# Optimization experiments

Measured on AMD Instinct MI355X. Metric: run time of the kernel, lower is better.

The kernel has to match this reference:

```python
import jax, jax.numpy as jnp
from jax import lax
import numpy as np

K = 48          # dim_embedding_key
PAST = 20
FUT = 40
N = 65536       # total surrounding-agent nodes
E = 1048576     # edges
B = 1           # batch (structurally forced to 1 by the original code)


def conv1d_relu(x, w, b):
    # x: [B, 2, T], w: [K, 2, 3], padding=1 -> relu(Conv1d)
    y = lax.conv_general_dilated(x, w, (1,), ((1, 1),),
                                 dimension_numbers=('NCH', 'OIH', 'NCH'))
    return jax.nn.relu(y + b[None, :, None])


def gru_cell(xt, h, Wih, Whh, bih, bhh):
    gi = xt @ Wih.T + bih
    gh = h @ Whh.T + bhh
    ir, iz, inn = jnp.split(gi, 3, axis=-1)
    hr, hz, hn = jnp.split(gh, 3, axis=-1)
    r = jax.nn.sigmoid(ir + hr)
    z = jax.nn.sigmoid(iz + hz)
    n = jnp.tanh(inn + r * hn)
    return (1 - z) * n + z * h


def gru_last(x, Wih, Whh, bih, bhh):
    # x: [Nb, T, Din]; returns final hidden state [Nb, H] (torch GRU, h0 = 0)
    h0 = jnp.zeros((x.shape[0], Whh.shape[1]), x.dtype)
    def step(h, xt):
        h2 = gru_cell(xt, h, Wih, Whh, bih, bhh)
        return h2, None
    hT, _ = lax.scan(step, h0, jnp.swapaxes(x, 0, 1))
    return hT


def gcn_conv(x, row, col, w, W, b, n):
    # PyG GCNConv(normalize=True): add self loops (weight 1), symmetric norm,
    # x @ W.T, gather at source `row`, scatter-add at target `col`, + bias.
    loop = jnp.arange(n)
    row = jnp.concatenate([row, loop])
    col = jnp.concatenate([col, loop])
    w = jnp.concatenate([w, jnp.ones((n,), w.dtype)])
    deg = jax.ops.segment_sum(w, col, num_segments=n)
    dinv = jnp.where(deg > 0, lax.rsqrt(jnp.where(deg > 0, deg, 1.0)), 0.0)
    norm = dinv[row] * w * dinv[col]
    xw = x @ W.T
    msg = xw[row] * norm[:, None]
    return jax.ops.segment_sum(msg, col, num_segments=n) + b


def forward(past, future, x, edge_index, edge_weight,
            conv_past_w, conv_past_b, conv_fut_w, conv_fut_b,
            enc_past_Wih, enc_past_Whh, enc_past_bih, enc_past_bhh,
            enc_fut_Wih, enc_fut_Whh, enc_fut_bih, enc_fut_bhh,
            dec_Wih, dec_Whh, dec_bih, dec_bhh,
            fc_w, fc_b, gcn1_w, gcn1_b, gcn2_w, gcn2_b):
    present0 = past[:, -1, :2]                                  # [B, 2]

    # --- surrounding agents: conv1d + GRU encoder over all N nodes ---
    inter_past = jnp.swapaxes(x.reshape(-1, PAST, 2), 1, 2)     # [N, 2, T]
    story_embed = jnp.swapaxes(conv1d_relu(inter_past, conv_past_w, conv_past_b), 1, 2)
    state_past = gru_last(story_embed, enc_past_Wih, enc_past_Whh, enc_past_bih, enc_past_bhh)  # [N, K]

    # --- GCN interaction (edge_weight nonempty branch); dropout is eval-mode identity ---
    ei = edge_index.reshape(2, -1)
    ew = edge_weight.reshape(-1)
    x1 = jax.nn.relu(gcn_conv(state_past, ei[0], ei[1], ew, gcn1_w, gcn1_b, N))
    x1 = gcn_conv(x1, ei[0], ei[1], ew, gcn2_w, gcn2_b, N)
    interact_past = x1[0].reshape(B, -1)                        # [B, K] (B == 1)

    # --- ego past / future encoders ---
    past_embed = jnp.swapaxes(conv1d_relu(jnp.swapaxes(past, 1, 2), conv_past_w, conv_past_b), 1, 2)
    fut_embed = jnp.swapaxes(conv1d_relu(jnp.swapaxes(future, 1, 2), conv_fut_w, conv_fut_b), 1, 2)
    target_past = gru_last(past_embed, enc_past_Wih, enc_past_Whh, enc_past_bih, enc_past_bhh)   # [B, K]
    state_fut = gru_last(fut_embed, enc_fut_Wih, enc_fut_Whh, enc_fut_bih, enc_fut_bhh)          # [B, K]

    state_conc = jnp.concatenate([interact_past, target_past, state_fut], axis=-1)               # [B, 3K]

    zeros_in = jnp.zeros_like(state_conc)
    def step(carry, i):
        h, present = carry
        inp = jnp.where(i == 0, state_conc, zeros_in)
        h = gru_cell(inp, h, dec_Wih, dec_Whh, dec_bih, dec_bhh)
        coords = present + h @ fc_w.T + fc_b
        return (h, coords), coords
    (_, _), coords_seq = lax.scan(step, (jnp.zeros((B, 3 * K), past.dtype), present0), jnp.arange(FUT))
    return jnp.swapaxes(coords_seq, 0, 1)                        # [B, FUT, 2]


def setup_inputs() -> dict:
    ks = jax.random.split(jax.random.key(0), 32)
    def p(k, shape, s=0.1):
        return jax.random.normal(k, shape, jnp.float32) * s
    inp = {
        'past': p(ks[0], (B, PAST, 2), 1.0),
        'future': p(ks[1], (B, FUT, 2), 1.0),
        'x': p(ks[2], (N, PAST, 2), 1.0),
        'edge_index': jax.random.randint(ks[3], (1, 2, E), 0, N, jnp.int32),
        'edge_weight': jax.random.uniform(ks[4], (1, E), jnp.float32),
        'conv_past_w': p(ks[5], (K, 2, 3)), 'conv_past_b': p(ks[6], (K,)),
        'conv_fut_w': p(ks[7], (K, 2, 3)), 'conv_fut_b': p(ks[8], (K,)),
        'enc_past_Wih': p(ks[9], (3 * K, K)), 'enc_past_Whh': p(ks[10], (3 * K, K)),
        'enc_past_bih': p(ks[11], (3 * K,)), 'enc_past_bhh': p(ks[12], (3 * K,)),
        'enc_fut_Wih': p(ks[13], (3 * K, K)), 'enc_fut_Whh': p(ks[14], (3 * K, K)),
        'enc_fut_bih': p(ks[15], (3 * K,)), 'enc_fut_bhh': p(ks[16], (3 * K,)),
        'dec_Wih': p(ks[17], (9 * K, 3 * K)), 'dec_Whh': p(ks[18], (9 * K, 3 * K)),
        'dec_bih': p(ks[19], (9 * K,)), 'dec_bhh': p(ks[20], (9 * K,)),
        'fc_w': p(ks[21], (2, 3 * K)), 'fc_b': p(ks[22], (2,)),
        'gcn1_w': p(ks[23], (K, K)), 'gcn1_b': p(ks[24], (K,)),
        'gcn2_w': p(ks[25], (K, K)), 'gcn2_b': p(ks[26], (K,)),
    }
    return inp


def reference(past, future, x, edge_index, edge_weight,
              conv_past_w, conv_past_b, conv_fut_w, conv_fut_b,
              enc_past_Wih, enc_past_Whh, enc_past_bih, enc_past_bhh,
              enc_fut_Wih, enc_fut_Whh, enc_fut_bih, enc_fut_bhh,
              dec_Wih, dec_Whh, dec_bih, dec_bhh,
              fc_w, fc_b, gcn1_w, gcn1_b, gcn2_w, gcn2_b):
    return forward(past, future, x, edge_index, edge_weight,
                   conv_past_w, conv_past_b, conv_fut_w, conv_fut_b,
                   enc_past_Wih, enc_past_Whh, enc_past_bih, enc_past_bhh,
                   enc_fut_Wih, enc_fut_Whh, enc_fut_bih, enc_fut_bhh,
                   dec_Wih, dec_Whh, dec_bih, dec_bhh,
                   fc_w, fc_b, gcn1_w, gcn1_b, gcn2_w, gcn2_b)
```

## Files before the change

kernel.cpp:

```cpp
#include <hip/hip_runtime.h>
#include <math.h>

#define NN 65536
#define NE 1048576
#define KH 48
#define G3 144
#define DEGB 512
#define PREPB 15
#define STAGEB 83

#define CAP_L1 8192
#define CAP_S1 4096
#define CAP_E2 65536
#define CAP_S2 8192

#define OFF_MARK1  0u
#define OFF_MARK2  262144u
#define OFF_CNT    524288u
#define OFF_L1R    524352u
#define OFF_L1W    557120u
#define OFF_S1G    589888u
#define OFF_E2R    606272u
#define OFF_E2S    868416u
#define OFF_E2W    1130560u
#define OFF_S2     1392704u
#define OFF_DEG2   1425472u
#define OFF_STATE  1458240u
#define OFF_X1     3031104u
#define OFF_TPSF   3817536u
#define OFF_WHH16  3818048u
#define OFF_GI0P   3947072u
#define OFF_GIP    3948800u
#define OFF_GIF    3960320u
#define OFF_DWH4   3983360u

typedef _Float16 h2_t __attribute__((ext_vector_type(2)));
typedef _Float16 h4_t __attribute__((ext_vector_type(4)));
typedef _Float16 h8_t __attribute__((ext_vector_type(8)));

__device__ __forceinline__ float sigmf(float x) { return 1.0f / (1.0f + __expf(-x)); }
__device__ __forceinline__ float tanhfast(float x) {
    float e = __expf(2.0f * x);
    return 1.0f - 2.0f / (e + 1.0f);
}

#if __has_builtin(__builtin_amdgcn_fdot2)
__device__ __forceinline__ float fdot2f(h2_t a, h2_t b, float c) {
    return __builtin_amdgcn_fdot2(a, b, c, false);
}
#else
__device__ __forceinline__ float fdot2f(h2_t a, h2_t b, float c) {
    return c + (float)a.x * (float)b.x + (float)a.y * (float)b.y;
}
#endif

__global__ void k_edges1(const int* ei, const float* ew,
                         int* mark1, unsigned* cnt, int* l1r, float* l1w,
                         const float* past, const float* future,
                         const float* cpw, const float* cpb,
                         const float* cfw, const float* cfb,
                         const float* epWih, const float* epbih,
                         const float* efWih, const float* efbih,
                         float* giP, float* giF) {
    if (blockIdx.x >= NE / 4 / 256) {
        int p = blockIdx.x - NE / 4 / 256;
        const float* xs; const float* cw; const float* cb;
        const float* Wih; const float* bih; float* gout;
        int T, s0;
        if (p < 5) { xs = past;   cw = cpw; cb = cpb; Wih = epWih; bih = epbih;
                     gout = giP; T = 20; s0 = p * 4; }
        else       { xs = future; cw = cfw; cb = cfb; Wih = efWih; bih = efbih;
                     gout = giF; T = 40; s0 = (p - 5) * 4; }
        __shared__ __align__(16) float s_x[80];
        __shared__ __align__(16) float s_e[4 * KH];
        int t = threadIdx.x;
        if (t < T * 2) s_x[t] = xs[t];
        __syncthreads();
        for (int idx = t; idx < 4 * KH; idx += 256) {
            int lt = idx / KH;
            int k = idx - lt * KH;
            int tt = s0 + lt;
            float acc = cb[k];
#pragma unroll
            for (int d = 0; d < 3; ++d) {
                int tau = tt + d - 1;
                if (tau >= 0 && tau < T) {
                    acc += cw[k * 6 + d] * s_x[tau * 2 + 0];
                    acc += cw[k * 6 + 3 + d] * s_x[tau * 2 + 1];
                }
            }
            s_e[lt * KH + k] = fmaxf(acc, 0.0f);
        }
        __syncthreads();
        for (int idx = t; idx < 4 * G3; idx += 256) {
            int lt = idx / G3;
            int row = idx - lt * G3;
            const float4* wp = reinterpret_cast<const float4*>(Wih + row * KH);
            const float4* em = reinterpret_cast<const float4*>(s_e + lt * KH);
            float g = bih[row];
#pragma unroll
            for (int j = 0; j < 12; ++j) {
                float4 w4 = wp[j]; float4 e4 = em[j];
                g += w4.x * e4.x + w4.y * e4.y + w4.z * e4.z + w4.w * e4.w;
            }
            gout[(s0 + lt) * G3 + row] = g;
        }
        return;
    }
    int q = blockIdx.x * blockDim.x + threadIdx.x;
    if (q >= NE / 4) return;
    if (q == 0) mark1[0] = 1;
    int4 c4 = reinterpret_cast<const int4*>(ei + NE)[q];
    int e = q * 4;
    int cc[4] = {c4.x, c4.y, c4.z, c4.w};
#pragma unroll
    for (int j = 0; j < 4; ++j) {
        if (cc[j] == 0) {
            int r = ei[e + j];
            float w = ew[e + j];
            unsigned s = atomicAdd(&cnt[0], 1u);
            if (s < CAP_L1) { l1r[s] = r; l1w[s] = w; }
            mark1[r] = 1;
        }
    }
}

__global__ void k_compact1(int* mark1, int* mark2, unsigned* cnt,
                           int* e2r, int* e2s, float* e2w, int* s1g,
                           float* x1, const float* g1b) {
    int i = blockIdx.x * blockDim.x + threadIdx.x;
    if (i >= NN) return;
    if (mark1[i]) {
        unsigned s = atomicAdd(&cnt[1], 1u);
        if (s < CAP_S1) {
            mark1[i] = (int)s + 1;
            mark2[i] = 1;
            s1g[s] = i;
            unsigned t = atomicAdd(&cnt[2], 1u);
            if (t < CAP_E2) { e2r[t] = i; e2s[t] = (int)s; e2w[t] = 1.0f; }
            for (int k = 0; k < KH; ++k) x1[s * KH + k] = g1b[k];
        } else {
            mark1[i] = 0;
        }
    }
}

__global__ void k_edges2(const int* ei, const float* ew,
                         const int* mark1, int* mark2, unsigned* cnt,
                         int* e2r, int* e2s, float* e2w) {
    int q = blockIdx.x * blockDim.x + threadIdx.x;
    if (q >= NE / 4) return;
    int4 c4 = reinterpret_cast<const int4*>(ei + NE)[q];
    int e = q * 4;
    int cc[4] = {c4.x, c4.y, c4.z, c4.w};
#pragma unroll
    for (int j = 0; j < 4; ++j) {
        int m = mark1[cc[j]];
        if (m > 0) {
            int r = ei[e + j];
            float w = ew[e + j];
            unsigned s = atomicAdd(&cnt[2], 1u);
            if (s < CAP_E2) { e2r[s] = r; e2s[s] = m - 1; e2w[s] = w; }
            mark2[r] = 1;
        }
    }
}

__global__ void k_compact2(int* mark2, unsigned* cnt, int* s2, float* deg2) {
    int i = blockIdx.x * blockDim.x + threadIdx.x;
    if (i >= NN) return;
    if (mark2[i]) {
        unsigned s = atomicAdd(&cnt[3], 1u);
        if (s < CAP_S2) { s2[s] = i; mark2[i] = (int)s + 1; deg2[s] = 1.0f; }
        else mark2[i] = 0;
    }
}

__device__ void gru_seq(const float* xseq, int T,
                        const float* cw, const float* cb,
                        const float* Wih, const float* Whh,
                        const float* bih, const float* bhh,
                        float* out48,
                        float* s_x, float* s_embed, float* s_giA,
                        float* s_h ) {
    int t = threadIdx.x;
    int nt = blockDim.x;
    for (int i = t; i < T * 2; i += nt) s_x[i] = xseq[i];
    __syncthreads();
    for (int idx = t; idx < T * KH; idx += nt) {
        int tt = idx / KH;
        int k = idx - tt * KH;
        float acc = cb[k];
#pragma unroll
        for (int d = 0; d < 3; ++d) {
            int tau = tt + d - 1;
            if (tau >= 0 && tau < T) {
                acc += cw[k * 6 + d] * s_x[tau * 2 + 0];
                acc += cw[k * 6 + 3 + d] * s_x[tau * 2 + 1];
            }
        }
        s_embed[tt * KH + k] = fmaxf(acc, 0.0f);
    }
    __syncthreads();
    for (int idx = t; idx < T * G3; idx += nt) {
        int step = idx / G3;
        int row = idx - step * G3;
        const float4* wp = reinterpret_cast<const float4*>(Wih + row * KH);
        const float4* em = reinterpret_cast<const float4*>(s_embed + step * KH);
        float g = bih[row];
#pragma unroll
        for (int j = 0; j < 12; ++j) {
            float4 w4 = wp[j]; float4 e4 = em[j];
            g += w4.x * e4.x + w4.y * e4.y + w4.z * e4.z + w4.w * e4.w;
        }
        s_giA[idx] = g;
    }
    int k = t >> 1, hf = t & 1;
    float4 wr[18];
    float bh0 = 0.0f, bh1 = 0.0f, bh2 = 0.0f;
    if (t < 96) {
#pragma unroll
        for (int g = 0; g < 3; ++g) {
            const float4* q = reinterpret_cast<const float4*>(
                Whh + (g * KH + k) * KH + hf * 24);
#pragma unroll
            for (int j = 0; j < 6; ++j) wr[g * 6 + j] = q[j];
        }
        if (hf == 0) { bh0 = bhh[k]; bh1 = bhh[KH + k]; bh2 = bhh[2 * KH + k]; }
    }
    if (t < KH) s_h[t] = 0.0f;
    float hk = 0.0f;
    for (int step = 0; step < T; ++step) {
        __syncthreads();
        int cur = step & 1, nxt = cur ^ 1;
        if (t < 96) {
            const float4* hp = reinterpret_cast<const float4*>(s_h + cur * KH)
                               + hf * 6;
            float a0 = bh0, a1 = bh1, a2 = bh2;
#pragma unroll
            for (int j = 0; j < 6; ++j) {
                float4 hv = hp[j];
                float4 w0 = wr[j], w1 = wr[6 + j], w2 = wr[12 + j];
                a0 += w0.x * hv.x + w0.y * hv.y + w0.z * hv.z + w0.w * hv.w;
                a1 += w1.x * hv.x + w1.y * hv.y + w1.z * hv.z + w1.w * hv.w;
                a2 += w2.x * hv.x + w2.y * hv.y + w2.z * hv.z + w2.w * hv.w;
            }
            a0 += __shfl_xor(a0, 1);
            a1 += __shfl_xor(a1, 1);
            a2 += __shfl_xor(a2, 1);
            if (hf == 0) {
                const float* gi = s_giA + step * G3;
                float r = sigmf(gi[k] + a0);
                float z = sigmf(gi[KH + k] + a1);
                float n = tanhfast(gi[2 * KH + k] + r * a2);
                hk = (1.0f - z) * n + z * hk;
                s_h[nxt * KH + k] = hk;
            }
        }
    }
    __syncthreads();
    if (t < KH) out48[t] = s_h[(T & 1) * KH + t];
}

__device__ void gru_rec(const float* giA , int T,
                        const float* Whh, const float* bhh,
                        float* out48, float* s_h ) {
    int t = threadIdx.x;
    int k = t >> 1, hf = t & 1;
    float4 wr[18];
    float bh0 = 0.0f, bh1 = 0.0f, bh2 = 0.0f;
    if (t < 96) {
#pragma unroll
        for (int g = 0; g < 3; ++g) {
            const float4* q = reinterpret_cast<const float4*>(
                Whh + (g * KH + k) * KH + hf * 24);
#pragma unroll
            for (int j = 0; j < 6; ++j) wr[g * 6 + j] = q[j];
        }
        if (hf == 0) { bh0 = bhh[k]; bh1 = bhh[KH + k]; bh2 = bhh[2 * KH + k]; }
    }
    if (t < KH) s_h[t] = 0.0f;
    float hk = 0.0f;
    for (int step = 0; step < T; ++step) {
        __syncthreads();
        int cur = step & 1, nxt = cur ^ 1;
        if (t < 96) {
            const float4* hp = reinterpret_cast<const float4*>(s_h + cur * KH)
                               + hf * 6;
            float a0 = bh0, a1 = bh1, a2 = bh2;
#pragma unroll
            for (int j = 0; j < 6; ++j) {
                float4 hv = hp[j];
                float4 w0 = wr[j], w1 = wr[6 + j], w2 = wr[12 + j];
                a0 += w0.x * hv.x + w0.y * hv.y + w0.z * hv.z + w0.w * hv.w;
                a1 += w1.x * hv.x + w1.y * hv.y + w1.z * hv.z + w1.w * hv.w;
                a2 += w2.x * hv.x + w2.y * hv.y + w2.z * hv.z + w2.w * hv.w;
            }
            a0 += __shfl_xor(a0, 1);
            a1 += __shfl_xor(a1, 1);
            a2 += __shfl_xor(a2, 1);
            if (hf == 0) {
                const float* gi = giA + step * G3;
                float r = sigmf(gi[k] + a0);
                float z = sigmf(gi[KH + k] + a1);
                float n = tanhfast(gi[2 * KH + k] + r * a2);
                hk = (1.0f - z) * n + z * hk;
                s_h[nxt * KH + k] = hk;
            }
        }
    }
    __syncthreads();
    if (t < KH) out48[t] = s_h[(T & 1) * KH + t];
}

__global__ __launch_bounds__(192, 2) void k_gru(
    const float* x, const float* cpw, const float* cpb,
    const float* epWih, const float* epWhh, const float* epbih, const float* epbhh,
    const float* efWhh, const float* efbhh,
    const float* giP, const float* giF,
    const int* ei, const float* ew, const int* mark2, float* deg2,
    const int* s2, const unsigned* cnt, float* state, float* tpsf) {
    if (blockIdx.x < DEGB) {
        int per = NE / DEGB;
        int lo = blockIdx.x * per;
        for (int e = lo + threadIdx.x; e < lo + per; e += blockDim.x) {
            int c = ei[NE + e];
            int m = mark2[c];
            if (m > 0) atomicAdd(&deg2[m - 1], ew[e]);
        }
        return;
    }
    __shared__ __align__(16) float s_x[80];
    __shared__ __align__(16) float s_embed[40 * KH];
    __shared__ __align__(16) float s_giA[40 * G3];
    __shared__ __align__(16) float s_h[2 * KH];
    if (blockIdx.x == DEGB) {
        gru_rec(giP, 20, epWhh, epbhh, tpsf, s_h);
        return;
    }
    if (blockIdx.x == DEGB + 1) {
        gru_rec(giF, 40, efWhh, efbhh, tpsf + 64, s_h);
        return;
    }
    int b0 = blockIdx.x - (DEGB + 2);
    int nw = gridDim.x - (DEGB + 2);
    int cnt2 = (int)min(cnt[3], (unsigned)CAP_S2);
    for (int b = b0; b < cnt2; b += nw) {
        int node = s2[b];
        gru_seq(x + (size_t)node * 40, 20, cpw, cpb, epWih, epWhh, epbih, epbhh,
                state + (size_t)b * KH, s_x, s_embed, s_giA, s_h);
    }
}

__global__ void k_acc1(const unsigned* cnt, const int* e2r, const int* e2s,
                       const float* e2w, const int* mark2, const float* deg2,
                       const int* s1g, const float* state,
                       const float* W1, float* x1,
                       const float* dWhh, const float* dWih,
                       const float* dbih, const float* tpsf,
                       _Float16* whh16, float* dwh4, float* gi0p) {
    if (blockIdx.x < STAGEB) {
        int id = blockIdx.x * blockDim.x + threadIdx.x;
        if (id < 27 * 576) {
            int c = id / 576, t = id - c * 576;
            int k = t >> 2, q = t & 3;
            int g = c / 9, u = c - g * 9;
            const float* src = dWhh + (size_t)(g * G3 + k) * G3 + q * 36 + 4 * u;
            float4 f = *reinterpret_cast<const float4*>(src);
            h2_t a, b;
            a.x = (_Float16)f.x; a.y = (_Float16)f.y;
            b.x = (_Float16)f.z; b.y = (_Float16)f.w;
            int pid = ((c >> 1) * 576 + t) * 2 + (c & 1);
            h2_t* o = reinterpret_cast<h2_t*>(whh16);
            o[2 * pid + 0] = a;
            o[2 * pid + 1] = b;
            return;
        }
        if (id < 27 * 576 + 9 * 576) {
            int id2 = id - 27 * 576;
            int c = id2 / 576, t = id2 - c * 576;
            int k = t >> 2, q = t & 3;
            int g = c / 3, j = c - g * 3;
            const float* src = dWih + (size_t)(g * G3 + k) * G3 + q * 12 + 4 * j;
            reinterpret_cast<float4*>(dwh4)[id2] =
                *reinterpret_cast<const float4*>(src);
            return;
        }
        int row = id - (27 * 576 + 9 * 576);
        if (row < 432) {
            const float* wr = dWih + (size_t)row * G3;
            float acc = dbih[row];
#pragma unroll
            for (int m = 0; m < 48; ++m) acc += wr[48 + m] * tpsf[m];
#pragma unroll
            for (int m = 0; m < 48; ++m) acc += wr[96 + m] * tpsf[64 + m];
            gi0p[row] = acc;
        }
        return;
    }
    int nE = (int)min(cnt[2], (unsigned)CAP_E2);
    int total = nE * KH;
    int stride = (gridDim.x - STAGEB) * blockDim.x;
    for (int idx = (blockIdx.x - STAGEB) * blockDim.x + threadIdx.x; idx < total;
         idx += stride) {
        int e = idx / KH;
        int k = idx - e * KH;
        int row = e2r[e];
        int s2i = mark2[row] - 1;
        if (s2i < 0) continue;
        int cglob = s1g[e2s[e]];
        int cs2 = mark2[cglob] - 1;
        float norm = e2w[e] * rsqrtf(deg2[s2i] * deg2[cs2]);
        const float* sp = state + (size_t)s2i * KH;
        const float* wp = W1 + k * KH;
        float acc = 0.0f;
#pragma unroll
        for (int m = 0; m < KH; ++m) acc += sp[m] * wp[m];
        atomicAdd(&x1[e2s[e] * KH + k], acc * norm);
    }
}

__global__ __launch_bounds__(640, 1) void k_dec(
    const unsigned* cnt, const int* l1r, const float* l1w,
    const int* mark1, const int* mark2, const float* deg2, const float* x1,
    const float* W2, const float* b2, const float* tpsf, const float* past,
    const _Float16* whh16, const float* dwh4, const float* gi0p,
    const float* dbih, const float* dbhh,
    const float* fcw, const float* fcb, float* out) {
    __shared__ __align__(16) float s_conc[G3];
    __shared__ __align__(16) _Float16 s_h16[2][G3];
    __shared__ __align__(16) float s_hf[2][G3];
    int t = threadIdx.x;
    int k = t >> 2, q = t & 3;
    h8_t wv[13];
    h4_t wv26 = (h4_t)(_Float16)0.0f;
    float4 dv[9];
    float bh[3] = {0.0f, 0.0f, 0.0f};
    float bi[3] = {0.0f, 0.0f, 0.0f};
#pragma unroll
    for (int c2 = 0; c2 < 13; ++c2) wv[c2] = (h8_t)(_Float16)0.0f;
#pragma unroll
    for (int j = 0; j < 9; ++j) dv[j] = make_float4(0.f, 0.f, 0.f, 0.f);
    if (t < 576) {
        const h8_t* wp8 = reinterpret_cast<const h8_t*>(whh16);
#pragma unroll
        for (int c2 = 0; c2 < 13; ++c2) wv[c2] = wp8[c2 * 576 + t];
        wv26 = reinterpret_cast<const h4_t*>(whh16)[(13 * 576 + t) * 2];
        const float4* dp = reinterpret_cast<const float4*>(dwh4);
#pragma unroll
        for (int j = 0; j < 9; ++j) dv[j] = dp[j * 576 + t];
        if (q == 0) {
#pragma unroll
            for (int g = 0; g < 3; ++g) {
                bh[g] = dbhh[g * G3 + k];
                bi[g] = dbih[g * G3 + k];
            }
        }
    }
    float fw0[3] = {0, 0, 0}, fw1[3] = {0, 0, 0};
    float fcb0 = 0.0f, fcb1 = 0.0f, pres0 = 0.0f, pres1 = 0.0f;
    if (t >= 576) {
        int lane = t - 576;
#pragma unroll
        for (int j = 0; j < 3; ++j) {
            int m = lane + 64 * j;
            if (m < G3) { fw0[j] = fcw[m]; fw1[j] = fcw[G3 + m]; }
        }
        if (lane == 0) {
            fcb0 = fcb[0]; fcb1 = fcb[1];
            pres0 = past[38]; pres1 = past[39];
        }
    }
    if (t < 48) s_conc[t] = b2[t];
    else if (t < 96) s_conc[t] = tpsf[t - 48];
    else if (t < 144) s_conc[t] = tpsf[64 + t - 96];
    if (t < G3) {
        s_h16[0][t] = (_Float16)0.0f;
        s_hf[0][t] = 0.0f;
    }
    __syncthreads();
    int cl1 = (int)min(cnt[0], (unsigned)CAP_L1);
    float dinv0 = rsqrtf(deg2[mark2[0] - 1]);
    int items = (cl1 + 1) * KH;
    for (int idx = t; idx < items; idx += blockDim.x) {
        int e = idx / KH;
        int kk = idx - e * KH;
        int row; float norm;
        if (e == cl1) { row = 0; norm = dinv0 * dinv0; }
        else {
            row = l1r[e];
            int rs2 = mark2[row] - 1;
            if (rs2 < 0) continue;
            norm = l1w[e] * rsqrtf(deg2[rs2]) * dinv0;
        }
        int s1 = mark1[row] - 1;
        if (s1 < 0) continue;
        const float* xp = x1 + (size_t)s1 * KH;
        const float* wp = W2 + kk * KH;
        float acc = 0.0f;
#pragma unroll
        for (int m = 0; m < KH; ++m) acc += fmaxf(xp[m], 0.0f) * wp[m];
        atomicAdd(&s_conc[kk], acc * norm);
    }
    h2_t wh[54];
    if (t < 576) {
#pragma unroll
        for (int c2 = 0; c2 < 13; ++c2) {
            h8_t v = wv[c2];
            int c0 = 2 * c2, c1 = 2 * c2 + 1;
            int g0 = c0 / 9, u0 = c0 - g0 * 9;
            int g1 = c1 / 9, u1 = c1 - g1 * 9;
            wh[g0 * 18 + 2 * u0]     = __builtin_shufflevector(v, v, 0, 1);
            wh[g0 * 18 + 2 * u0 + 1] = __builtin_shufflevector(v, v, 2, 3);
            wh[g1 * 18 + 2 * u1]     = __builtin_shufflevector(v, v, 4, 5);
            wh[g1 * 18 + 2 * u1 + 1] = __builtin_shufflevector(v, v, 6, 7);
        }
        wh[2 * 18 + 2 * 8]     = __builtin_shufflevector(wv26, wv26, 0, 1);
        wh[2 * 18 + 2 * 8 + 1] = __builtin_shufflevector(wv26, wv26, 2, 3);
    } else {
#pragma unroll
        for (int j = 0; j < 54; ++j) wh[j] = (h2_t)(_Float16)0.0f;
    }
    __syncthreads();
    float gi0[3] = {0.0f, 0.0f, 0.0f};
    if (t < 576) {
        const float4* cc = reinterpret_cast<const float4*>(s_conc) + q * 3;
        float4 c0 = cc[0], c1 = cc[1], c2v = cc[2];
#pragma unroll
        for (int g = 0; g < 3; ++g) {
            float4 w0 = dv[g * 3 + 0];
            float4 w1 = dv[g * 3 + 1];
            float4 w2 = dv[g * 3 + 2];
            float acc = w0.x * c0.x + w0.y * c0.y + w0.z * c0.z + w0.w * c0.w;
            acc += w1.x * c1.x + w1.y * c1.y + w1.z * c1.z + w1.w * c1.w;
            acc += w2.x * c2v.x + w2.y * c2v.y + w2.z * c2v.z + w2.w * c2v.w;
            acc += __shfl_xor(acc, 1);
            acc += __shfl_xor(acc, 2);
            gi0[g] = acc + gi0p[g * G3 + k];
        }
    }
    float hk = 0.0f;
    for (int i = 0; i < 40; ++i) {
        __syncthreads();
        int cur = i & 1, nxt = cur ^ 1;
        if (t < 576) {
            const h4_t* hp = reinterpret_cast<const h4_t*>(&s_h16[cur][0]) + q * 9;
            float a0 = bh[0], a1 = bh[1], a2 = bh[2];
#pragma unroll
            for (int j = 0; j < 9; ++j) {
                h4_t hv = hp[j];
                h2_t lo = __builtin_shufflevector(hv, hv, 0, 1);
                h2_t hi = __builtin_shufflevector(hv, hv, 2, 3);
                a0 = fdot2f(wh[2 * j], lo, a0);
                a1 = fdot2f(wh[18 + 2 * j], lo, a1);
                a2 = fdot2f(wh[36 + 2 * j], lo, a2);
                a0 = fdot2f(wh[2 * j + 1], hi, a0);
                a1 = fdot2f(wh[18 + 2 * j + 1], hi, a1);
                a2 = fdot2f(wh[36 + 2 * j + 1], hi, a2);
            }
            a0 += __shfl_xor(a0, 1); a0 += __shfl_xor(a0, 2);
            a1 += __shfl_xor(a1, 1); a1 += __shfl_xor(a1, 2);
            a2 += __shfl_xor(a2, 1); a2 += __shfl_xor(a2, 2);
            if (q == 0) {
                float gr = ((i == 0) ? gi0[0] : bi[0]) + a0;
                float gz = ((i == 0) ? gi0[1] : bi[1]) + a1;
                float gn = ((i == 0) ? gi0[2] : bi[2]);
                float r = sigmf(gr);
                float z = sigmf(gz);
                float n = tanhfast(gn + r * a2);
                hk = (1.0f - z) * n + z * hk;
                s_h16[nxt][k] = (_Float16)hk;
                s_hf[nxt][k] = hk;
            }
        } else if (i >= 1) {
            int lane = t - 576;
            const float* hsrc = s_hf[cur];
            float p0 = 0.0f, p1 = 0.0f;
#pragma unroll
            for (int j = 0; j < 3; ++j) {
                int m = lane + 64 * j;
                if (m < G3) { float h = hsrc[m]; p0 += h * fw0[j]; p1 += h * fw1[j]; }
            }
#pragma unroll
            for (int off = 32; off > 0; off >>= 1) {
                p0 += __shfl_down(p0, off);
                p1 += __shfl_down(p1, off);
            }
            if (lane == 0) {
                pres0 += p0 + fcb0; pres1 += p1 + fcb1;
                out[(i - 1) * 2 + 0] = pres0;
                out[(i - 1) * 2 + 1] = pres1;
            }
        }
    }
    __syncthreads();
    if (t >= 576) {
        int lane = t - 576;
        const float* hsrc = s_hf[0];
        float p0 = 0.0f, p1 = 0.0f;
#pragma unroll
        for (int j = 0; j < 3; ++j) {
            int m = lane + 64 * j;
            if (m < G3) { float h = hsrc[m]; p0 += h * fw0[j]; p1 += h * fw1[j]; }
        }
#pragma unroll
        for (int off = 32; off > 0; off >>= 1) {
            p0 += __shfl_down(p0, off);
            p1 += __shfl_down(p1, off);
        }
        if (lane == 0) {
            pres0 += p0 + fcb0; pres1 += p1 + fcb1;
            out[39 * 2 + 0] = pres0;
            out[39 * 2 + 1] = pres1;
        }
    }
}

extern "C" void kernel_launch(void* const* d_in, const int* in_sizes, int n_in,
                              void* d_out, int out_size, void* d_ws, size_t ws_size,
                              hipStream_t stream) {
    (void)in_sizes; (void)n_in; (void)out_size; (void)ws_size;
    const float* past   = (const float*)d_in[0];
    const float* future = (const float*)d_in[1];
    const float* x      = (const float*)d_in[2];
    const int*   ei     = (const int*)d_in[3];
    const float* ew     = (const float*)d_in[4];
    const float* cpw    = (const float*)d_in[5];
    const float* cpb    = (const float*)d_in[6];
    const float* cfw    = (const float*)d_in[7];
    const float* cfb    = (const float*)d_in[8];
    const float* epWih  = (const float*)d_in[9];
    const float* epWhh  = (const float*)d_in[10];
    const float* epbih  = (const float*)d_in[11];
    const float* epbhh  = (const float*)d_in[12];
    const float* efWih  = (const float*)d_in[13];
    const float* efWhh  = (const float*)d_in[14];
    const float* efbih  = (const float*)d_in[15];
    const float* efbhh  = (const float*)d_in[16];
    const float* dWih   = (const float*)d_in[17];
    const float* dWhh   = (const float*)d_in[18];
    const float* dbih   = (const float*)d_in[19];
    const float* dbhh   = (const float*)d_in[20];
    const float* fcw    = (const float*)d_in[21];
    const float* fcb    = (const float*)d_in[22];
    const float* g1w    = (const float*)d_in[23];
    const float* g1b    = (const float*)d_in[24];
    const float* g2w    = (const float*)d_in[25];
    const float* g2b    = (const float*)d_in[26];

    char* ws = (char*)d_ws;
    int*      mark1 = (int*)(ws + OFF_MARK1);
    int*      mark2 = (int*)(ws + OFF_MARK2);
    unsigned* cnt   = (unsigned*)(ws + OFF_CNT);
    int*      l1r   = (int*)(ws + OFF_L1R);
    float*    l1w   = (float*)(ws + OFF_L1W);
    int*      s1g   = (int*)(ws + OFF_S1G);
    int*      e2r   = (int*)(ws + OFF_E2R);
    int*      e2s   = (int*)(ws + OFF_E2S);
    float*    e2w   = (float*)(ws + OFF_E2W);
    int*      s2    = (int*)(ws + OFF_S2);
    float*    deg2  = (float*)(ws + OFF_DEG2);
    float*    state = (float*)(ws + OFF_STATE);
    float*    x1    = (float*)(ws + OFF_X1);
    float*    tpsf  = (float*)(ws + OFF_TPSF);
    _Float16* whh16 = (_Float16*)(ws + OFF_WHH16);
    float*    gi0p  = (float*)(ws + OFF_GI0P);
    float*    giP   = (float*)(ws + OFF_GIP);
    float*    giF   = (float*)(ws + OFF_GIF);
    float*    dwh4  = (float*)(ws + OFF_DWH4);

    hipMemsetAsync(ws, 0, 524352, stream);
    k_edges1<<<NE / 4 / 256 + PREPB, 256, 0, stream>>>(
        ei, ew, mark1, cnt, l1r, l1w,
        past, future, cpw, cpb, cfw, cfb,
        epWih, epbih, efWih, efbih, giP, giF);
    k_compact1<<<NN / 256, 256, 0, stream>>>(mark1, mark2, cnt, e2r, e2s, e2w, s1g, x1, g1b);
    k_edges2<<<NE / 4 / 256, 256, 0, stream>>>(ei, ew, mark1, mark2, cnt, e2r, e2s, e2w);
    k_compact2<<<NN / 256, 256, 0, stream>>>(mark2, cnt, s2, deg2);
    k_gru<<<DEGB + 2 + 512, 192, 0, stream>>>(x, cpw, cpb, epWih, epWhh, epbih, epbhh,
                                              efWhh, efbhh, giP, giF,
                                              ei, ew, mark2, deg2,
                                              s2, cnt, state, tpsf);
    k_acc1<<<STAGEB + 128, 256, 0, stream>>>(cnt, e2r, e2s, e2w, mark2, deg2, s1g,
                                             state, g1w, x1,
                                             dWhh, dWih, dbih, tpsf,
                                             whh16, dwh4, gi0p);
    k_dec<<<1, 640, 0, stream>>>(cnt, l1r, l1w, mark1, mark2, deg2, x1, g2w, g2b,
                                 tpsf, past, whh16, dwh4, gi0p, dbih, dbhh, fcw, fcb,
                                 (float*)d_out);
}
```

Measured before the change: 213.0 us.

## Fuse node compaction into edge scans with atomic claim, drop compact kernels

Removes the two full-node compaction kernels. Nodes are now claimed inline during the edge scans through an atomicAdd slot reservation followed by atomicCAS on the mark arrays. The decoder weight repacking moves from k_acc1 into spare blocks of k_edges2, so it runs alongside the edge scan. Two fewer launches and 65536-element passes, at the cost of possibly wasted s2 slots (marked -1 and skipped in k_gru), a less deterministic ordering, and more atomics in the hot edge loops.

After: 212.4 us. About the same (-0.3%).

```diff
diff --git a/kernel.cpp b/kernel.cpp
--- a/kernel.cpp
+++ b/kernel.cpp
@@ -7,7 +7,9 @@
 #define G3 144
 #define DEGB 512
 #define PREPB 15
-#define STAGEB 83
+#define E1B 1024
+#define SB2 81
+#define GIB 2
 
 #define CAP_L1 8192
 #define CAP_S1 4096
@@ -54,16 +56,46 @@
 }
 #endif
 
+__device__ __forceinline__ void s2_append(int r, unsigned* cnt, int* mark2,
+                                          int* s2, float* deg2) {
+    if (mark2[r] != 0) return;
+    unsigned idx = atomicAdd(&cnt[3], 1u);
+    if (idx >= CAP_S2) return;
+    int old = atomicCAS(&mark2[r], 0, (int)idx + 1);
+    deg2[idx] = 1.0f;
+    s2[idx] = (old == 0) ? r : -1;
+}
+
+__device__ __forceinline__ void s1_claim(int r, unsigned* cnt, int* mark1,
+                                         int* mark2, int* s1g,
+                                         int* e2r, int* e2s, float* e2w,
+                                         float* x1, const float* g1b,
+                                         int* s2, float* deg2) {
+    if (mark1[r] != 0) return;
+    unsigned idx = atomicAdd(&cnt[1], 1u);
+    if (idx >= CAP_S1) return;
+    int old = atomicCAS(&mark1[r], 0, (int)idx + 1);
+    if (old != 0) return;
+    s1g[idx] = r;
+    unsigned t2 = atomicAdd(&cnt[2], 1u);
+    if (t2 < CAP_E2) { e2r[t2] = r; e2s[t2] = (int)idx; e2w[t2] = 1.0f; }
+    for (int k = 0; k < KH; ++k) x1[idx * KH + k] = g1b[k];
+    s2_append(r, cnt, mark2, s2, deg2);
+}
+
 __global__ void k_edges1(const int* ei, const float* ew,
-                         int* mark1, unsigned* cnt, int* l1r, float* l1w,
+                         int* mark1, int* mark2, unsigned* cnt,
+                         int* l1r, float* l1w, int* s1g,
+                         int* e2r, int* e2s, float* e2w,
+                         float* x1, const float* g1b, int* s2, float* deg2,
                          const float* past, const float* future,
                          const float* cpw, const float* cpb,
                          const float* cfw, const float* cfb,
                          const float* epWih, const float* epbih,
                          const float* efWih, const float* efbih,
                          float* giP, float* giF) {
-    if (blockIdx.x >= NE / 4 / 256) {
-        int p = blockIdx.x - NE / 4 / 256;
+    if (blockIdx.x >= E1B) {
+        int p = blockIdx.x - E1B;
         const float* xs; const float* cw; const float* cb;
         const float* Wih; const float* bih; float* gout;
         int T, s0;
@@ -108,8 +140,8 @@
         return;
     }
     int q = blockIdx.x * blockDim.x + threadIdx.x;
-    if (q >= NE / 4) return;
-    if (q == 0) mark1[0] = 1;
+    if (q == 0)
+        s1_claim(0, cnt, mark1, mark2, s1g, e2r, e2s, e2w, x1, g1b, s2, deg2);
     int4 c4 = reinterpret_cast<const int4*>(ei + NE)[q];
     int e = q * 4;
     int cc[4] = {c4.x, c4.y, c4.z, c4.w};
@@ -120,35 +152,45 @@
             float w = ew[e + j];
             unsigned s = atomicAdd(&cnt[0], 1u);
             if (s < CAP_L1) { l1r[s] = r; l1w[s] = w; }
-            mark1[r] = 1;
-        }
-    }
-}
-
-__global__ void k_compact1(int* mark1, int* mark2, unsigned* cnt,
-                           int* e2r, int* e2s, float* e2w, int* s1g,
-                           float* x1, const float* g1b) {
-    int i = blockIdx.x * blockDim.x + threadIdx.x;
-    if (i >= NN) return;
-    if (mark1[i]) {
-        unsigned s = atomicAdd(&cnt[1], 1u);
-        if (s < CAP_S1) {
-            mark1[i] = (int)s + 1;
-            mark2[i] = 1;
-            s1g[s] = i;
-            unsigned t = atomicAdd(&cnt[2], 1u);
-            if (t < CAP_E2) { e2r[t] = i; e2s[t] = (int)s; e2w[t] = 1.0f; }
-            for (int k = 0; k < KH; ++k) x1[s * KH + k] = g1b[k];
-        } else {
-            mark1[i] = 0;
+            s1_claim(r, cnt, mark1, mark2, s1g, e2r, e2s, e2w, x1, g1b, s2, deg2);
         }
     }
 }
 
 __global__ void k_edges2(const int* ei, const float* ew,
                          const int* mark1, int* mark2, unsigned* cnt,
-                         int* e2r, int* e2s, float* e2w) {
-    int q = blockIdx.x * blockDim.x + threadIdx.x;
+                         int* e2r, int* e2s, float* e2w, int* s2, float* deg2,
+                         const float* dWhh, const float* dWih,
+                         _Float16* whh16, float* dwh4) {
+    if (blockIdx.x < SB2) {
+        int id = blockIdx.x * blockDim.x + threadIdx.x;
+        if (id < 27 * 576) {
+            int c = id / 576, t = id - c * 576;
+            int k = t >> 2, q = t & 3;
+            int g = c / 9, u = c - g * 9;
+            const float* src = dWhh + (size_t)(g * G3 + k) * G3 + q * 36 + 4 * u;
+            float4 f = *reinterpret_cast<const float4*>(src);
+            h2_t a, b;
+            a.x = (_Float16)f.x; a.y = (_Float16)f.y;
+            b.x = (_Float16)f.z; b.y = (_Float16)f.w;
+            int pid = ((c >> 1) * 576 + t) * 2 + (c & 1);
+            h2_t* o = reinterpret_cast<h2_t*>(whh16);
+            o[2 * pid + 0] = a;
+            o[2 * pid + 1] = b;
+            return;
+        }
+        int id2 = id - 27 * 576;
+        if (id2 < 9 * 576) {
+            int c = id2 / 576, t = id2 - c * 576;
+            int k = t >> 2, q = t & 3;
+            int g = c / 3, j = c - g * 3;
+            const float* src = dWih + (size_t)(g * G3 + k) * G3 + q * 12 + 4 * j;
+            reinterpret_cast<float4*>(dwh4)[id2] =
+                *reinterpret_cast<const float4*>(src);
+        }
+        return;
+    }
+    int q = (blockIdx.x - SB2) * blockDim.x + threadIdx.x;
     if (q >= NE / 4) return;
     int4 c4 = reinterpret_cast<const int4*>(ei + NE)[q];
     int e = q * 4;
@@ -161,18 +203,8 @@
             float w = ew[e + j];
             unsigned s = atomicAdd(&cnt[2], 1u);
             if (s < CAP_E2) { e2r[s] = r; e2s[s] = m - 1; e2w[s] = w; }
-            mark2[r] = 1;
-        }
-    }
-}
-
-__global__ void k_compact2(int* mark2, unsigned* cnt, int* s2, float* deg2) {
-    int i = blockIdx.x * blockDim.x + threadIdx.x;
-    if (i >= NN) return;
-    if (mark2[i]) {
-        unsigned s = atomicAdd(&cnt[3], 1u);
-        if (s < CAP_S2) { s2[s] = i; mark2[i] = (int)s + 1; deg2[s] = 1.0f; }
-        else mark2[i] = 0;
+            s2_append(r, cnt, mark2, s2, deg2);
+        }
     }
 }
 
@@ -347,6 +379,7 @@
     int cnt2 = (int)min(cnt[3], (unsigned)CAP_S2);
     for (int b = b0; b < cnt2; b += nw) {
         int node = s2[b];
+        if (node < 0) continue;
         gru_seq(x + (size_t)node * 40, 20, cpw, cpb, epWih, epWhh, epbih, epbhh,
                 state + (size_t)b * KH, s_x, s_embed, s_giA, s_h);
     }
@@ -356,37 +389,10 @@
                        const float* e2w, const int* mark2, const float* deg2,
                        const int* s1g, const float* state,
                        const float* W1, float* x1,
-                       const float* dWhh, const float* dWih,
-                       const float* dbih, const float* tpsf,
-                       _Float16* whh16, float* dwh4, float* gi0p) {
-    if (blockIdx.x < STAGEB) {
-        int id = blockIdx.x * blockDim.x + threadIdx.x;
-        if (id < 27 * 576) {
-            int c = id / 576, t = id - c * 576;
-            int k = t >> 2, q = t & 3;
-            int g = c / 9, u = c - g * 9;
-            const float* src = dWhh + (size_t)(g * G3 + k) * G3 + q * 36 + 4 * u;
-            float4 f = *reinterpret_cast<const float4*>(src);
-            h2_t a, b;
-            a.x = (_Float16)f.x; a.y = (_Float16)f.y;
-            b.x = (_Float16)f.z; b.y = (_Float16)f.w;
-            int pid = ((c >> 1) * 576 + t) * 2 + (c & 1);
-            h2_t* o = reinterpret_cast<h2_t*>(whh16);
-            o[2 * pid + 0] = a;
-            o[2 * pid + 1] = b;
-            return;
-        }
-        if (id < 27 * 576 + 9 * 576) {
-            int id2 = id - 27 * 576;
-            int c = id2 / 576, t = id2 - c * 576;
-            int k = t >> 2, q = t & 3;
-            int g = c / 3, j = c - g * 3;
-            const float* src = dWih + (size_t)(g * G3 + k) * G3 + q * 12 + 4 * j;
-            reinterpret_cast<float4*>(dwh4)[id2] =
-                *reinterpret_cast<const float4*>(src);
-            return;
-        }
-        int row = id - (27 * 576 + 9 * 576);
+                       const float* dWih, const float* dbih, const float* tpsf,
+                       float* gi0p) {
+    if (blockIdx.x < GIB) {
+        int row = blockIdx.x * blockDim.x + threadIdx.x;
         if (row < 432) {
             const float* wr = dWih + (size_t)row * G3;
             float acc = dbih[row];
@@ -400,8 +406,8 @@
     }
     int nE = (int)min(cnt[2], (unsigned)CAP_E2);
     int total = nE * KH;
-    int stride = (gridDim.x - STAGEB) * blockDim.x;
-    for (int idx = (blockIdx.x - STAGEB) * blockDim.x + threadIdx.x; idx < total;
+    int stride = (gridDim.x - GIB) * blockDim.x;
+    for (int idx = (blockIdx.x - GIB) * blockDim.x + threadIdx.x; idx < total;
          idx += stride) {
         int e = idx / KH;
         int k = idx - e * KH;
@@ -670,21 +676,21 @@
     float*    dwh4  = (float*)(ws + OFF_DWH4);
 
     hipMemsetAsync(ws, 0, 524352, stream);
-    k_edges1<<<NE / 4 / 256 + PREPB, 256, 0, stream>>>(
-        ei, ew, mark1, cnt, l1r, l1w,
+    k_edges1<<<E1B + PREPB, 256, 0, stream>>>(
+        ei, ew, mark1, mark2, cnt, l1r, l1w, s1g, e2r, e2s, e2w,
+        x1, g1b, s2, deg2,
         past, future, cpw, cpb, cfw, cfb,
         epWih, epbih, efWih, efbih, giP, giF);
-    k_compact1<<<NN / 256, 256, 0, stream>>>(mark1, mark2, cnt, e2r, e2s, e2w, s1g, x1, g1b);
-    k_edges2<<<NE / 4 / 256, 256, 0, stream>>>(ei, ew, mark1, mark2, cnt, e2r, e2s, e2w);
-    k_compact2<<<NN / 256, 256, 0, stream>>>(mark2, cnt, s2, deg2);
+    k_edges2<<<SB2 + E1B, 256, 0, stream>>>(ei, ew, mark1, mark2, cnt,
+                                            e2r, e2s, e2w, s2, deg2,
+                                            dWhh, dWih, whh16, dwh4);
     k_gru<<<DEGB + 2 + 512, 192, 0, stream>>>(x, cpw, cpb, epWih, epWhh, epbih, epbhh,
                                               efWhh, efbhh, giP, giF,
                                               ei, ew, mark2, deg2,
                                               s2, cnt, state, tpsf);
-    k_acc1<<<STAGEB + 128, 256, 0, stream>>>(cnt, e2r, e2s, e2w, mark2, deg2, s1g,
-                                             state, g1w, x1,
-                                             dWhh, dWih, dbih, tpsf,
-                                             whh16, dwh4, gi0p);
+    k_acc1<<<GIB + 128, 256, 0, stream>>>(cnt, e2r, e2s, e2w, mark2, deg2, s1g,
+                                          state, g1w, x1,
+                                          dWih, dbih, tpsf, gi0p);
     k_dec<<<1, 640, 0, stream>>>(cnt, l1r, l1w, mark1, mark2, deg2, x1, g2w, g2b,
                                  tpsf, past, whh16, dwh4, gi0p, dbih, dbhh, fcw, fcb,
                                  (float*)d_out);
```
